# Kernel tuning notes

Hardware: AMD Instinct MI355X
Metric: run time of the kernel (lower is better)

## Reference

```python
import jax, jax.numpy as jnp
import numpy as np

N, D, H, O = 512, 128, 256, 256

def setup_inputs() -> dict:
    key = jax.random.key(0)
    ks = jax.random.split(key, 10)
    s = lambda fan_in: 1.0 / np.sqrt(fan_in)
    return {
        "x": jax.random.normal(ks[0], (N, D), dtype=jnp.float32),
        "adj": jax.random.uniform(ks[1], (N, N), dtype=jnp.float32),
        # mpnn_compute: MLP(2D -> H -> H)
        "W1": jax.random.normal(ks[2], (H, 2 * D), dtype=jnp.float32) * s(2 * D),
        "b1": jnp.zeros((H,), dtype=jnp.float32),
        "W2": jax.random.normal(ks[3], (H, H), dtype=jnp.float32) * s(H),
        "b2": jnp.zeros((H,), dtype=jnp.float32),
        # out_compute: MLP(H -> H -> O)
        "Wo1": jax.random.normal(ks[4], (H, H), dtype=jnp.float32) * s(H),
        "bo1": jnp.zeros((H,), dtype=jnp.float32),
        "Wo2": jax.random.normal(ks[5], (O, H), dtype=jnp.float32) * s(H),
        "bo2": jnp.zeros((O,), dtype=jnp.float32),
    }


def reference(x, adj, W1, b1, W2, b2, Wo1, bo1, Wo2, bo2):
    n, d = x.shape
    # e[i, j] = concat(x[j], x[i]); split W1 so we never materialize the cat:
    # linear_1(e)[i,j] = x[j] @ Wa^T + x[i] @ Wb^T + b1
    Wa = W1[:, :d]   # acts on x[j] (first half of cat = x1 = x broadcast over i)
    Wb = W1[:, d:]   # acts on x[i] (second half = x2)
    pa = x @ Wa.T    # [N, H], indexed by j
    pb = x @ Wb.T    # [N, H], indexed by i
    h = jax.nn.relu(pa[None, :, :] + pb[:, None, :] + b1)  # [N, N, H]
    e = jnp.einsum('ijh,kh->ijk', h, W2) + b2               # [N, N, H]
    pred = jnp.mean(adj[:, :, None] * e, axis=1)            # [N, H]
    # out_compute MLP (normalize_input=False)
    h2 = jax.nn.relu(pred @ Wo1.T + bo1)
    return h2 @ Wo2.T + bo2                                  # [N, O]
```

## Files before the change

### kernel.cpp

```cpp
#include <hip/hip_runtime.h>

#define NN 512
#define DD 128
#define HH 256

__device__ __forceinline__ float dot4(float4 a, float4 b) {
    return a.x * b.x + a.y * b.y + a.z * b.z + a.w * b.w;
}

__global__ __launch_bounds__(256) void k1_pre(const float* __restrict__ x,
                                              const float* __restrict__ W1,
                                              const float* __restrict__ b1,
                                              const float* __restrict__ W2,
                                              const float* __restrict__ Wo1,
                                              const float* __restrict__ Wo2,
                                              float* __restrict__ pa,
                                              float* __restrict__ pbb,
                                              float* __restrict__ wsT) {
    __shared__ float smem[64 * 68];
    const int b = blockIdx.x;
    const int t = threadIdx.x;
    if (b < 256) {
        float (*xs)[DD] = (float(*)[DD])smem;
        const int i0 = b * 2;
        if (t < 64) {
            const int f = t * 4;
            *(float4*)&xs[f >> 7][f & 127] = *(const float4*)&x[i0 * DD + f];
        }
        __syncthreads();
        const int h = t;
        const float4* w4 = (const float4*)(W1 + h * (2 * DD));
        const float4* x0 = (const float4*)&xs[0][0];
        const float4* x1 = (const float4*)&xs[1][0];
        float a0 = 0.f, a1 = 0.f, c0 = 0.f, c1 = 0.f;
        #pragma unroll 8
        for (int d4 = 0; d4 < DD / 4; ++d4) {
            float4 wa = w4[d4];
            float4 wb = w4[d4 + 32];
            float4 v0 = x0[d4];
            float4 v1 = x1[d4];
            a0 += dot4(wa, v0);
            a1 += dot4(wa, v1);
            c0 += dot4(wb, v0);
            c1 += dot4(wb, v1);
        }
        const float bb = b1[h];
        pa[i0 * HH + h] = a0;
        pa[(i0 + 1) * HH + h] = a1;
        pbb[i0 * HH + h] = c0 + bb;
        pbb[(i0 + 1) * HH + h] = c1 + bb;
    } else {
        float (*tl)[68] = (float(*)[68])smem;
        const int bb = b - 256;
        const int m = bb >> 4, tile = bb & 15;
        const float* src = (m == 0) ? W2 : (m == 1) ? Wo1 : Wo2;
        float* dst = wsT + m * (HH * HH);
        const int sr0 = (tile >> 2) * 64;
        const int sc0 = (tile & 3) * 64;
        const int rr = t >> 4;
        const int cc = (t & 15) * 4;
        #pragma unroll
        for (int it = 0; it < 4; ++it) {
            const int row = rr + 16 * it;
            float4 v = *(const float4*)&src[(sr0 + row) * HH + sc0 + cc];
            tl[row][cc + 0] = v.x;
            tl[row][cc + 1] = v.y;
            tl[row][cc + 2] = v.z;
            tl[row][cc + 3] = v.w;
        }
        __syncthreads();
        #pragma unroll
        for (int it = 0; it < 4; ++it) {
            const int lc = rr + 16 * it;
            float4 o;
            o.x = tl[cc + 0][lc];
            o.y = tl[cc + 1][lc];
            o.z = tl[cc + 2][lc];
            o.w = tl[cc + 3][lc];
            *(float4*)&dst[(sc0 + lc) * HH + sr0 + cc] = o;
        }
    }
}

__global__ __launch_bounds__(1024) void k2_rest(const float* __restrict__ adj,
                                                const float* __restrict__ pa,
                                                const float* __restrict__ pbb,
                                                const float* __restrict__ wsT,
                                                const float* __restrict__ b2,
                                                const float* __restrict__ bo1,
                                                const float* __restrict__ bo2,
                                                float* __restrict__ out) {
    __shared__ float adjs[2][NN];
    __shared__ float pbbs[2][HH];
    __shared__ float ts[2][HH];
    __shared__ float buf1[2][HH];
    __shared__ float buf2[2][HH];
    __shared__ float redbuf[4096];
    __shared__ float rsum_s[2];

    const int b = blockIdx.x;
    const int t = threadIdx.x;
    const int i0 = b * 2;

    if (t < 256) {
        const int f = t * 4;
        *(float4*)&adjs[f >> 9][f & 511] = *(const float4*)&adj[(i0 + (f >> 9)) * NN + (f & 511)];
    } else if (t < 384) {
        const int f = (t - 256) * 4;
        *(float4*)&pbbs[f >> 8][f & 255] = *(const float4*)&pbb[(i0 + (f >> 8)) * HH + (f & 255)];
    }
    __syncthreads();

    if (t < 128) {
        const int r = t >> 6, l = t & 63;
        float s = 0.f;
        #pragma unroll
        for (int m = 0; m < 8; ++m) s += adjs[r][l + 64 * m];
        #pragma unroll
        for (int off = 32; off > 0; off >>= 1) s += __shfl_down(s, off, 64);
        if (l == 0) rsum_s[r] = s;
    }

    {
        const int hb = t >> 9;
        const int jq = (t >> 7) & 3;
        const int hl = t & 127;
        const int h = hb * 128 + hl;
        const float pb0 = pbbs[0][h];
        const float pb1 = pbbs[1][h];
        float ac0 = 0.f, ac1 = 0.f;
        const float* pac = pa + (jq * 128) * HH + h;
        #pragma unroll 4
        for (int j = 0; j < 128; j += 4) {
            float p0 = pac[(j + 0) * HH];
            float p1 = pac[(j + 1) * HH];
            float p2 = pac[(j + 2) * HH];
            float p3 = pac[(j + 3) * HH];
            float4 A0 = *(const float4*)&adjs[0][jq * 128 + j];
            float4 A1 = *(const float4*)&adjs[1][jq * 128 + j];
            ac0 += A0.x * fmaxf(p0 + pb0, 0.f);
            ac0 += A0.y * fmaxf(p1 + pb0, 0.f);
            ac0 += A0.z * fmaxf(p2 + pb0, 0.f);
            ac0 += A0.w * fmaxf(p3 + pb0, 0.f);
            ac1 += A1.x * fmaxf(p0 + pb1, 0.f);
            ac1 += A1.y * fmaxf(p1 + pb1, 0.f);
            ac1 += A1.z * fmaxf(p2 + pb1, 0.f);
            ac1 += A1.w * fmaxf(p3 + pb1, 0.f);
        }
        redbuf[((jq * 2 + hb) * 2 + 0) * 128 + hl] = ac0;
        redbuf[((jq * 2 + hb) * 2 + 1) * 128 + hl] = ac1;
        __syncthreads();
        if (jq == 0) {
            #pragma unroll
            for (int r = 0; r < 2; ++r) {
                float s = (r == 0 ? ac0 : ac1);
                #pragma unroll
                for (int q = 1; q < 4; ++q)
                    s += redbuf[((q * 2 + hb) * 2 + r) * 128 + hl];
                ts[r][h] = s;
            }
        }
    }
    __syncthreads();

    const int k = t & 255;
    const int hp = t >> 8;
    const float* W2T  = wsT;
    const float* Wo1T = wsT + HH * HH;
    const float* Wo2T = wsT + 2 * HH * HH;

    {
        const float* wt = W2T + (hp * 64) * HH + k;
        float a0 = 0.f, a1 = 0.f;
        #pragma unroll 8
        for (int hh = 0; hh < 64; ++hh) {
            float w = wt[hh * HH];
            a0 += w * ts[0][hp * 64 + hh];
            a1 += w * ts[1][hp * 64 + hh];
        }
        redbuf[(hp * 2 + 0) * 256 + k] = a0;
        redbuf[(hp * 2 + 1) * 256 + k] = a1;
        __syncthreads();
        if (hp == 0) {
            const float bv = b2[k];
            const float inv = 1.0f / (float)NN;
            float s0 = a0, s1 = a1;
            #pragma unroll
            for (int p = 1; p < 4; ++p) {
                s0 += redbuf[(p * 2 + 0) * 256 + k];
                s1 += redbuf[(p * 2 + 1) * 256 + k];
            }
            buf1[0][k] = (s0 + bv * rsum_s[0]) * inv;
            buf1[1][k] = (s1 + bv * rsum_s[1]) * inv;
        }
    }
    __syncthreads();

    {
        const float* wt = Wo1T + (hp * 64) * HH + k;
        float a0 = 0.f, a1 = 0.f;
        #pragma unroll 8
        for (int hh = 0; hh < 64; ++hh) {
            float w = wt[hh * HH];
            a0 += w * buf1[0][hp * 64 + hh];
            a1 += w * buf1[1][hp * 64 + hh];
        }
        redbuf[(hp * 2 + 0) * 256 + k] = a0;
        redbuf[(hp * 2 + 1) * 256 + k] = a1;
        __syncthreads();
        if (hp == 0) {
            const float bv = bo1[k];
            float s0 = a0, s1 = a1;
            #pragma unroll
            for (int p = 1; p < 4; ++p) {
                s0 += redbuf[(p * 2 + 0) * 256 + k];
                s1 += redbuf[(p * 2 + 1) * 256 + k];
            }
            buf2[0][k] = fmaxf(s0 + bv, 0.f);
            buf2[1][k] = fmaxf(s1 + bv, 0.f);
        }
    }
    __syncthreads();

    {
        const float* wt = Wo2T + (hp * 64) * HH + k;
        float a0 = 0.f, a1 = 0.f;
        #pragma unroll 8
        for (int hh = 0; hh < 64; ++hh) {
            float w = wt[hh * HH];
            a0 += w * buf2[0][hp * 64 + hh];
            a1 += w * buf2[1][hp * 64 + hh];
        }
        redbuf[(hp * 2 + 0) * 256 + k] = a0;
        redbuf[(hp * 2 + 1) * 256 + k] = a1;
        __syncthreads();
        if (hp == 0) {
            const float bv = bo2[k];
            float s0 = a0, s1 = a1;
            #pragma unroll
            for (int p = 1; p < 4; ++p) {
                s0 += redbuf[(p * 2 + 0) * 256 + k];
                s1 += redbuf[(p * 2 + 1) * 256 + k];
            }
            out[i0 * HH + k] = s0 + bv;
            out[(i0 + 1) * HH + k] = s1 + bv;
        }
    }
}

extern "C" void kernel_launch(void* const* d_in, const int* in_sizes, int n_in,
                              void* d_out, int out_size, void* d_ws, size_t ws_size,
                              hipStream_t stream) {
    const float* x   = (const float*)d_in[0];
    const float* adj = (const float*)d_in[1];
    const float* W1  = (const float*)d_in[2];
    const float* b1  = (const float*)d_in[3];
    const float* W2  = (const float*)d_in[4];
    const float* b2  = (const float*)d_in[5];
    const float* Wo1 = (const float*)d_in[6];
    const float* bo1 = (const float*)d_in[7];
    const float* Wo2 = (const float*)d_in[8];
    const float* bo2 = (const float*)d_in[9];
    float* out = (float*)d_out;
    float* ws  = (float*)d_ws;

    float* pa  = ws;
    float* pbb = ws + 131072;
    float* wsT = ws + 262144;

    k1_pre<<<304, 256, 0, stream>>>(x, W1, b1, W2, Wo1, Wo2, pa, pbb, wsT);
    k2_rest<<<256, 1024, 0, stream>>>(adj, pa, pbb, wsT, b2, bo1, bo2, out);
}
```

Measured before the change: 36.77 us.

## Transpose W1 for coalesced pa/pb projection and rotate loop starts per block

W1 is now transposed in a separate kernel, together with the other weight matrices, so the projection kernel reads weights coalesced across threads instead of one strided row per thread. The pa/pb projection, the adjacency-weighted aggregation and the three MLP stages each get a per-block rotated start offset, which spreads cache and channel accesses across blocks. Accumulation is split into even/odd partial sums to shorten dependency chains. The cost is one extra kernel launch and a serialized transpose-then-project dependency, and the sums are reordered.

```diff
diff --git a/kernel.cpp b/kernel.cpp
--- a/kernel.cpp
+++ b/kernel.cpp
@@ -4,82 +4,114 @@
 #define DD 128
 #define HH 256
 
-__device__ __forceinline__ float dot4(float4 a, float4 b) {
-    return a.x * b.x + a.y * b.y + a.z * b.z + a.w * b.w;
-}
-
-__global__ __launch_bounds__(256) void k1_pre(const float* __restrict__ x,
-                                              const float* __restrict__ W1,
-                                              const float* __restrict__ b1,
-                                              const float* __restrict__ W2,
-                                              const float* __restrict__ Wo1,
-                                              const float* __restrict__ Wo2,
-                                              float* __restrict__ pa,
-                                              float* __restrict__ pbb,
-                                              float* __restrict__ wsT) {
-    __shared__ float smem[64 * 68];
+__global__ __launch_bounds__(256) void k0_tr(const float* __restrict__ W1,
+                                             const float* __restrict__ W2,
+                                             const float* __restrict__ Wo1,
+                                             const float* __restrict__ Wo2,
+                                             float* __restrict__ wsT) {
+    __shared__ float tl[64][68];
     const int b = blockIdx.x;
     const int t = threadIdx.x;
-    if (b < 256) {
-        float (*xs)[DD] = (float(*)[DD])smem;
-        const int i0 = b * 2;
-        if (t < 64) {
-            const int f = t * 4;
-            *(float4*)&xs[f >> 7][f & 127] = *(const float4*)&x[i0 * DD + f];
-        }
-        __syncthreads();
-        const int h = t;
-        const float4* w4 = (const float4*)(W1 + h * (2 * DD));
-        const float4* x0 = (const float4*)&xs[0][0];
-        const float4* x1 = (const float4*)&xs[1][0];
-        float a0 = 0.f, a1 = 0.f, c0 = 0.f, c1 = 0.f;
-        #pragma unroll 8
-        for (int d4 = 0; d4 < DD / 4; ++d4) {
-            float4 wa = w4[d4];
-            float4 wb = w4[d4 + 32];
-            float4 v0 = x0[d4];
-            float4 v1 = x1[d4];
-            a0 += dot4(wa, v0);
-            a1 += dot4(wa, v1);
-            c0 += dot4(wb, v0);
-            c1 += dot4(wb, v1);
-        }
-        const float bb = b1[h];
-        pa[i0 * HH + h] = a0;
-        pa[(i0 + 1) * HH + h] = a1;
-        pbb[i0 * HH + h] = c0 + bb;
-        pbb[(i0 + 1) * HH + h] = c1 + bb;
-    } else {
-        float (*tl)[68] = (float(*)[68])smem;
-        const int bb = b - 256;
-        const int m = bb >> 4, tile = bb & 15;
-        const float* src = (m == 0) ? W2 : (m == 1) ? Wo1 : Wo2;
-        float* dst = wsT + m * (HH * HH);
-        const int sr0 = (tile >> 2) * 64;
-        const int sc0 = (tile & 3) * 64;
-        const int rr = t >> 4;
-        const int cc = (t & 15) * 4;
-        #pragma unroll
-        for (int it = 0; it < 4; ++it) {
-            const int row = rr + 16 * it;
-            float4 v = *(const float4*)&src[(sr0 + row) * HH + sc0 + cc];
-            tl[row][cc + 0] = v.x;
-            tl[row][cc + 1] = v.y;
-            tl[row][cc + 2] = v.z;
-            tl[row][cc + 3] = v.w;
-        }
-        __syncthreads();
-        #pragma unroll
-        for (int it = 0; it < 4; ++it) {
-            const int lc = rr + 16 * it;
-            float4 o;
-            o.x = tl[cc + 0][lc];
-            o.y = tl[cc + 1][lc];
-            o.z = tl[cc + 2][lc];
-            o.w = tl[cc + 3][lc];
-            *(float4*)&dst[(sc0 + lc) * HH + sr0 + cc] = o;
-        }
-    }
+    const int m = b >> 4, tile = b & 15;
+    const float* src = (m == 0) ? W1 : (m == 1) ? W2 : (m == 2) ? Wo1 : Wo2;
+    float* dst = wsT + m * (HH * HH);
+    const int sr0 = (tile >> 2) * 64;
+    const int sc0 = (tile & 3) * 64;
+    const int rr = t >> 4;
+    const int cc = (t & 15) * 4;
+    #pragma unroll
+    for (int it = 0; it < 4; ++it) {
+        const int row = rr + 16 * it;
+        float4 v = *(const float4*)&src[(sr0 + row) * HH + sc0 + cc];
+        tl[row][cc + 0] = v.x;
+        tl[row][cc + 1] = v.y;
+        tl[row][cc + 2] = v.z;
+        tl[row][cc + 3] = v.w;
+    }
+    __syncthreads();
+    #pragma unroll
+    for (int it = 0; it < 4; ++it) {
+        const int lc = rr + 16 * it;
+        float4 o;
+        o.x = tl[cc + 0][lc];
+        o.y = tl[cc + 1][lc];
+        o.z = tl[cc + 2][lc];
+        o.w = tl[cc + 3][lc];
+        *(float4*)&dst[(sc0 + lc) * HH + sr0 + cc] = o;
+    }
+}
+
+__global__ __launch_bounds__(256) void k1_papb(const float* __restrict__ x,
+                                               const float* __restrict__ W1T,
+                                               const float* __restrict__ b1,
+                                               float* __restrict__ pa,
+                                               float* __restrict__ pbb) {
+    __shared__ float xs[2][DD];
+    const int b = blockIdx.x;
+    const int t = threadIdx.x;
+    const int i0 = b * 2;
+    if (t < 64) {
+        const int f = t * 4;
+        *(float4*)&xs[f >> 7][f & 127] = *(const float4*)&x[i0 * DD + f];
+    }
+    __syncthreads();
+    const float* wt = W1T + t;
+    const int crot = (b * 8) & 127;
+    float pe0 = 0.f, po0 = 0.f, pe1 = 0.f, po1 = 0.f;
+    float qe0 = 0.f, qo0 = 0.f, qe1 = 0.f, qo1 = 0.f;
+    #pragma unroll 2
+    for (int cc0 = 0; cc0 < 128; cc0 += 8) {
+        const int c = (cc0 + crot) & 127;
+        float w0 = wt[(c + 0) * HH], w1 = wt[(c + 1) * HH];
+        float w2 = wt[(c + 2) * HH], w3 = wt[(c + 3) * HH];
+        float w4 = wt[(c + 4) * HH], w5 = wt[(c + 5) * HH];
+        float w6 = wt[(c + 6) * HH], w7 = wt[(c + 7) * HH];
+        float v0 = wt[(128 + c + 0) * HH], v1 = wt[(128 + c + 1) * HH];
+        float v2 = wt[(128 + c + 2) * HH], v3 = wt[(128 + c + 3) * HH];
+        float v4 = wt[(128 + c + 4) * HH], v5 = wt[(128 + c + 5) * HH];
+        float v6 = wt[(128 + c + 6) * HH], v7 = wt[(128 + c + 7) * HH];
+        float4 x0a = *(const float4*)&xs[0][c];
+        float4 x0b = *(const float4*)&xs[0][c + 4];
+        float4 x1a = *(const float4*)&xs[1][c];
+        float4 x1b = *(const float4*)&xs[1][c + 4];
+        pe0 += w0 * x0a.x + w1 * x0a.y + w2 * x0a.z + w3 * x0a.w;
+        po0 += w4 * x0b.x + w5 * x0b.y + w6 * x0b.z + w7 * x0b.w;
+        pe1 += w0 * x1a.x + w1 * x1a.y + w2 * x1a.z + w3 * x1a.w;
+        po1 += w4 * x1b.x + w5 * x1b.y + w6 * x1b.z + w7 * x1b.w;
+        qe0 += v0 * x0a.x + v1 * x0a.y + v2 * x0a.z + v3 * x0a.w;
+        qo0 += v4 * x0b.x + v5 * x0b.y + v6 * x0b.z + v7 * x0b.w;
+        qe1 += v0 * x1a.x + v1 * x1a.y + v2 * x1a.z + v3 * x1a.w;
+        qo1 += v4 * x1b.x + v5 * x1b.y + v6 * x1b.z + v7 * x1b.w;
+    }
+    const float bb = b1[t];
+    pa[i0 * HH + t] = pe0 + po0;
+    pa[(i0 + 1) * HH + t] = pe1 + po1;
+    pbb[i0 * HH + t] = qe0 + qo0 + bb;
+    pbb[(i0 + 1) * HH + t] = qe1 + qo1 + bb;
+}
+
+__device__ __forceinline__ void stage_dot8(const float* __restrict__ wt,
+                                           const float* in0, const float* in1,
+                                           int hrot, float& A0, float& A1) {
+    float e0 = 0.f, o0 = 0.f, e1 = 0.f, o1 = 0.f;
+    #pragma unroll 2
+    for (int hh0 = 0; hh0 < 64; hh0 += 8) {
+        const int hh = (hh0 + hrot) & 63;
+        float w0 = wt[(hh + 0) * HH], w1 = wt[(hh + 1) * HH];
+        float w2 = wt[(hh + 2) * HH], w3 = wt[(hh + 3) * HH];
+        float w4 = wt[(hh + 4) * HH], w5 = wt[(hh + 5) * HH];
+        float w6 = wt[(hh + 6) * HH], w7 = wt[(hh + 7) * HH];
+        float4 t0a = *(const float4*)&in0[hh];
+        float4 t0b = *(const float4*)&in0[hh + 4];
+        float4 t1a = *(const float4*)&in1[hh];
+        float4 t1b = *(const float4*)&in1[hh + 4];
+        e0 += w0 * t0a.x + w1 * t0a.y + w2 * t0a.z + w3 * t0a.w;
+        o0 += w4 * t0b.x + w5 * t0b.y + w6 * t0b.z + w7 * t0b.w;
+        e1 += w0 * t1a.x + w1 * t1a.y + w2 * t1a.z + w3 * t1a.w;
+        o1 += w4 * t1b.x + w5 * t1b.y + w6 * t1b.z + w7 * t1b.w;
+    }
+    A0 = e0 + o0;
+    A1 = e1 + o1;
 }
 
 __global__ __launch_bounds__(1024) void k2_rest(const float* __restrict__ adj,
@@ -128,25 +160,37 @@
         const int h = hb * 128 + hl;
         const float pb0 = pbbs[0][h];
         const float pb1 = pbbs[1][h];
-        float ac0 = 0.f, ac1 = 0.f;
         const float* pac = pa + (jq * 128) * HH + h;
-        #pragma unroll 4
-        for (int j = 0; j < 128; j += 4) {
-            float p0 = pac[(j + 0) * HH];
-            float p1 = pac[(j + 1) * HH];
-            float p2 = pac[(j + 2) * HH];
-            float p3 = pac[(j + 3) * HH];
-            float4 A0 = *(const float4*)&adjs[0][jq * 128 + j];
-            float4 A1 = *(const float4*)&adjs[1][jq * 128 + j];
-            ac0 += A0.x * fmaxf(p0 + pb0, 0.f);
-            ac0 += A0.y * fmaxf(p1 + pb0, 0.f);
-            ac0 += A0.z * fmaxf(p2 + pb0, 0.f);
-            ac0 += A0.w * fmaxf(p3 + pb0, 0.f);
-            ac1 += A1.x * fmaxf(p0 + pb1, 0.f);
-            ac1 += A1.y * fmaxf(p1 + pb1, 0.f);
-            ac1 += A1.z * fmaxf(p2 + pb1, 0.f);
-            ac1 += A1.w * fmaxf(p3 + pb1, 0.f);
-        }
+        const float* arow0 = &adjs[0][jq * 128];
+        const float* arow1 = &adjs[1][jq * 128];
+        const int jrot = (b * 8) & 127;
+        float ae0 = 0.f, ao0 = 0.f, ae1 = 0.f, ao1 = 0.f;
+        #pragma unroll 2
+        for (int jj0 = 0; jj0 < 128; jj0 += 8) {
+            const int j = (jj0 + jrot) & 127;
+            float p0 = pac[(j + 0) * HH], p1 = pac[(j + 1) * HH];
+            float p2 = pac[(j + 2) * HH], p3 = pac[(j + 3) * HH];
+            float p4 = pac[(j + 4) * HH], p5 = pac[(j + 5) * HH];
+            float p6 = pac[(j + 6) * HH], p7 = pac[(j + 7) * HH];
+            float4 A0a = *(const float4*)&arow0[j];
+            float4 A0b = *(const float4*)&arow0[j + 4];
+            float4 A1a = *(const float4*)&arow1[j];
+            float4 A1b = *(const float4*)&arow1[j + 4];
+            float r0 = fmaxf(p0 + pb0, 0.f), r1 = fmaxf(p1 + pb0, 0.f);
+            float r2 = fmaxf(p2 + pb0, 0.f), r3 = fmaxf(p3 + pb0, 0.f);
+            float r4 = fmaxf(p4 + pb0, 0.f), r5 = fmaxf(p5 + pb0, 0.f);
+            float r6 = fmaxf(p6 + pb0, 0.f), r7 = fmaxf(p7 + pb0, 0.f);
+            ae0 += A0a.x * r0 + A0a.y * r1 + A0a.z * r2 + A0a.w * r3;
+            ao0 += A0b.x * r4 + A0b.y * r5 + A0b.z * r6 + A0b.w * r7;
+            float s0 = fmaxf(p0 + pb1, 0.f), s1 = fmaxf(p1 + pb1, 0.f);
+            float s2 = fmaxf(p2 + pb1, 0.f), s3 = fmaxf(p3 + pb1, 0.f);
+            float s4 = fmaxf(p4 + pb1, 0.f), s5 = fmaxf(p5 + pb1, 0.f);
+            float s6 = fmaxf(p6 + pb1, 0.f), s7 = fmaxf(p7 + pb1, 0.f);
+            ae1 += A1a.x * s0 + A1a.y * s1 + A1a.z * s2 + A1a.w * s3;
+            ao1 += A1b.x * s4 + A1b.y * s5 + A1b.z * s6 + A1b.w * s7;
+        }
+        const float ac0 = ae0 + ao0;
+        const float ac1 = ae1 + ao1;
         redbuf[((jq * 2 + hb) * 2 + 0) * 128 + hl] = ac0;
         redbuf[((jq * 2 + hb) * 2 + 1) * 128 + hl] = ac1;
         __syncthreads();
@@ -165,19 +209,14 @@
 
     const int k = t & 255;
     const int hp = t >> 8;
-    const float* W2T  = wsT;
-    const float* Wo1T = wsT + HH * HH;
-    const float* Wo2T = wsT + 2 * HH * HH;
+    const int hrot = (b * 8) & 63;
+    const float* W2T  = wsT + 1 * (HH * HH);
+    const float* Wo1T = wsT + 2 * (HH * HH);
+    const float* Wo2T = wsT + 3 * (HH * HH);
 
     {
-        const float* wt = W2T + (hp * 64) * HH + k;
-        float a0 = 0.f, a1 = 0.f;
-        #pragma unroll 8
-        for (int hh = 0; hh < 64; ++hh) {
-            float w = wt[hh * HH];
-            a0 += w * ts[0][hp * 64 + hh];
-            a1 += w * ts[1][hp * 64 + hh];
-        }
+        float a0, a1;
+        stage_dot8(W2T + (hp * 64) * HH + k, &ts[0][hp * 64], &ts[1][hp * 64], hrot, a0, a1);
         redbuf[(hp * 2 + 0) * 256 + k] = a0;
         redbuf[(hp * 2 + 1) * 256 + k] = a1;
         __syncthreads();
@@ -197,14 +236,8 @@
     __syncthreads();
 
     {
-        const float* wt = Wo1T + (hp * 64) * HH + k;
-        float a0 = 0.f, a1 = 0.f;
-        #pragma unroll 8
-        for (int hh = 0; hh < 64; ++hh) {
-            float w = wt[hh * HH];
-            a0 += w * buf1[0][hp * 64 + hh];
-            a1 += w * buf1[1][hp * 64 + hh];
-        }
+        float a0, a1;
+        stage_dot8(Wo1T + (hp * 64) * HH + k, &buf1[0][hp * 64], &buf1[1][hp * 64], hrot, a0, a1);
         redbuf[(hp * 2 + 0) * 256 + k] = a0;
         redbuf[(hp * 2 + 1) * 256 + k] = a1;
         __syncthreads();
@@ -223,14 +256,8 @@
     __syncthreads();
 
     {
-        const float* wt = Wo2T + (hp * 64) * HH + k;
-        float a0 = 0.f, a1 = 0.f;
-        #pragma unroll 8
-        for (int hh = 0; hh < 64; ++hh) {
-            float w = wt[hh * HH];
-            a0 += w * buf2[0][hp * 64 + hh];
-            a1 += w * buf2[1][hp * 64 + hh];
-        }
+        float a0, a1;
+        stage_dot8(Wo2T + (hp * 64) * HH + k, &buf2[0][hp * 64], &buf2[1][hp * 64], hrot, a0, a1);
         redbuf[(hp * 2 + 0) * 256 + k] = a0;
         redbuf[(hp * 2 + 1) * 256 + k] = a1;
         __syncthreads();
@@ -264,10 +291,11 @@
     float* out = (float*)d_out;
     float* ws  = (float*)d_ws;
 
-    float* pa  = ws;
-    float* pbb = ws + 131072;
-    float* wsT = ws + 262144;
-
-    k1_pre<<<304, 256, 0, stream>>>(x, W1, b1, W2, Wo1, Wo2, pa, pbb, wsT);
+    float* wsT = ws;
+    float* pa  = ws + 262144;
+    float* pbb = ws + 393216;
+
+    k0_tr<<<64, 256, 0, stream>>>(W1, W2, Wo1, Wo2, wsT);
+    k1_papb<<<256, 256, 0, stream>>>(x, wsT, b1, pa, pbb);
     k2_rest<<<256, 1024, 0, stream>>>(adj, pa, pbb, wsT, b2, bo1, bo2, out);
 }
```

New measurement: 32.62 us. 1.13x faster.
